# Kernel optimization log

Hardware: AMD Instinct MI355X
Metric: run time of the kernel (lower is better)

The kernel has to match this reference:

```python
import jax, jax.numpy as jnp
import numpy as np

B, D, P, K = 16384, 2048, 64, 5


def setup_inputs() -> dict:
    key = jax.random.key(0)
    k1, k2, k3, k4, k5 = jax.random.split(key, 5)
    s = 1.0 / np.sqrt(D)
    return {
        "x": jax.random.normal(k1, (B, D), dtype=jnp.float32),
        "parent_W": jax.random.normal(k2, (P, D), dtype=jnp.float32) * s,
        "parent_b": jax.random.normal(k3, (P,), dtype=jnp.float32) * s,
        "child_W": jax.random.normal(k4, (P, K, D), dtype=jnp.float32) * s,
        "child_b": jax.random.normal(k5, (P, K), dtype=jnp.float32) * s,
    }


def reference(x, parent_W, parent_b, child_W, child_b):
    # Parent linear: [B, P]
    parent_logits = x @ parent_W.T + parent_b
    # softmax is monotonic, so argmax(softmax(l)) == argmax(l)
    parent_class = jnp.argmax(parent_logits, axis=1)  # [B] int
    # Gather each sample's expert (child classifier) weights: [B, K, D], [B, K]
    Wc = child_W[parent_class]
    bc = child_b[parent_class]
    # Per-sample tiny GEMM, batched: [B, K]
    child_logits = jnp.einsum("bd,bkd->bk", x, Wc) + bc
    return parent_logits, child_logits
```

## Files before the change

### kernel.cpp

```cpp
#include <hip/hip_runtime.h>

#define B_ 16384
#define D_ 2048
#define P_ 64
#define K_ 5

#define BK 64
#define NCH (D_ / BK)
#define LDR 72
#define SPLIT_SC 2048.0f
#define SPLIT_INV (1.0f / 2048.0f)

typedef _Float16 half8 __attribute__((ext_vector_type(8)));
typedef float f32x4 __attribute__((ext_vector_type(4)));

static __device__ __forceinline__ void split8(const float4 a, const float4 b,
                                              half8& hi, half8& lo) {
  const float v[8] = {a.x, a.y, a.z, a.w, b.x, b.y, b.z, b.w};
#pragma unroll
  for (int i = 0; i < 8; ++i) {
    const _Float16 h = (_Float16)v[i];
    hi[i] = h;
    lo[i] = (_Float16)((v[i] - (float)h) * SPLIT_SC);
  }
}

__global__ __launch_bounds__(256) void k1_parent(
    const float* __restrict__ x, const float* __restrict__ pW,
    const float* __restrict__ pb, float* __restrict__ pout,
    int* __restrict__ cnt, int* __restrict__ list) {
  __shared__ _Float16 xlh[2][64 * LDR], xll[2][64 * LDR];
  __shared__ _Float16 wlh[2][64 * LDR], wll[2][64 * LDR];
  __shared__ float rmax[64][4];
  __shared__ int ridx[64][4];

  const int tid = threadIdx.x;
  const int b0 = blockIdx.x * 64;
  const int w = tid >> 6;
  const int l = tid & 63;
  const int r = tid >> 2;
  const int c = tid & 3;

  const float* xg = x + (size_t)(b0 + r) * D_ + c * 16;
  const float* wg = pW + (size_t)r * D_ + c * 16;
  const float bias = pb[w * 16 + (l & 15)];

  const int aoff = (l & 15) * LDR + (l >> 4) * 8;
  const int boff = (w * 16 + (l & 15)) * LDR + (l >> 4) * 8;
  const int soff = r * LDR + c * 16;

  f32x4 acc[4], accc[4];
#pragma unroll
  for (int fm = 0; fm < 4; ++fm) {
    acc[fm] = {0.f, 0.f, 0.f, 0.f};
    accc[fm] = {0.f, 0.f, 0.f, 0.f};
  }

  {
    const float4* xp = (const float4*)xg;
    const float4* wp = (const float4*)wg;
    half8 h, lo;
    split8(xp[0], xp[1], h, lo);
    *(half8*)&xlh[0][soff] = h; *(half8*)&xll[0][soff] = lo;
    split8(xp[2], xp[3], h, lo);
    *(half8*)&xlh[0][soff + 8] = h; *(half8*)&xll[0][soff + 8] = lo;
    split8(wp[0], wp[1], h, lo);
    *(half8*)&wlh[0][soff] = h; *(half8*)&wll[0][soff] = lo;
    split8(wp[2], wp[3], h, lo);
    *(half8*)&wlh[0][soff + 8] = h; *(half8*)&wll[0][soff + 8] = lo;
  }
  __syncthreads();

  for (int ch = 0; ch < NCH; ++ch) {
    const int cur = ch & 1;
    float4 x0, x1, x2, x3, w0, w1, w2, w3;
    const bool more = (ch + 1 < NCH);
    if (more) {
      const float4* xp = (const float4*)(xg + (ch + 1) * BK);
      const float4* wp = (const float4*)(wg + (ch + 1) * BK);
      x0 = xp[0]; x1 = xp[1]; x2 = xp[2]; x3 = xp[3];
      w0 = wp[0]; w1 = wp[1]; w2 = wp[2]; w3 = wp[3];
    }
#pragma unroll
    for (int s = 0; s < 2; ++s) {
      const int ko = s * 32;
      const half8 bh = *(const half8*)&wlh[cur][boff + ko];
      const half8 bl = *(const half8*)&wll[cur][boff + ko];
#pragma unroll
      for (int fm = 0; fm < 4; ++fm) {
        const half8 ah = *(const half8*)&xlh[cur][aoff + fm * 16 * LDR + ko];
        const half8 al = *(const half8*)&xll[cur][aoff + fm * 16 * LDR + ko];
        acc[fm]  = __builtin_amdgcn_mfma_f32_16x16x32_f16(ah, bh, acc[fm], 0, 0, 0);
        accc[fm] = __builtin_amdgcn_mfma_f32_16x16x32_f16(ah, bl, accc[fm], 0, 0, 0);
        accc[fm] = __builtin_amdgcn_mfma_f32_16x16x32_f16(al, bh, accc[fm], 0, 0, 0);
      }
    }
    if (more) {
      const int nxt = cur ^ 1;
      half8 h, lo;
      split8(x0, x1, h, lo);
      *(half8*)&xlh[nxt][soff] = h; *(half8*)&xll[nxt][soff] = lo;
      split8(x2, x3, h, lo);
      *(half8*)&xlh[nxt][soff + 8] = h; *(half8*)&xll[nxt][soff + 8] = lo;
      split8(w0, w1, h, lo);
      *(half8*)&wlh[nxt][soff] = h; *(half8*)&wll[nxt][soff] = lo;
      split8(w2, w3, h, lo);
      *(half8*)&wlh[nxt][soff + 8] = h; *(half8*)&wll[nxt][soff + 8] = lo;
    }
    __syncthreads();
  }

  const int colbase = w * 16 + (l & 15);
  float val[4][4];
#pragma unroll
  for (int fm = 0; fm < 4; ++fm) {
#pragma unroll
    for (int j = 0; j < 4; ++j) {
      val[fm][j] = acc[fm][j] + accc[fm][j] * SPLIT_INV + bias;
      const int row = fm * 16 + ((l >> 4) << 2) + j;
      pout[(size_t)(b0 + row) * P_ + colbase] = val[fm][j];
    }
  }
#pragma unroll
  for (int fm = 0; fm < 4; ++fm) {
#pragma unroll
    for (int j = 0; j < 4; ++j) {
      float bv = val[fm][j];
      int bi = colbase;
#pragma unroll
      for (int s = 8; s > 0; s >>= 1) {
        const float ov = __shfl_xor(bv, s, 64);
        const int oi = __shfl_xor(bi, s, 64);
        if (ov > bv || (ov == bv && oi < bi)) { bv = ov; bi = oi; }
      }
      if ((l & 15) == 0) {
        const int row = fm * 16 + ((l >> 4) << 2) + j;
        rmax[row][w] = bv;
        ridx[row][w] = bi;
      }
    }
  }
  __syncthreads();
  if (tid < 64) {
    float bv = rmax[tid][0];
    int bi = ridx[tid][0];
#pragma unroll
    for (int ww = 1; ww < 4; ++ww) {
      const float ov = rmax[tid][ww];
      const int oi = ridx[tid][ww];
      if (ov > bv || (ov == bv && oi < bi)) { bv = ov; bi = oi; }
    }
    const int slot = atomicAdd(&cnt[bi * 16], 1);
    if (slot < 1024) list[bi * 1024 + slot] = b0 + tid;
  }
}

__global__ __launch_bounds__(256) void k2_child(const float* __restrict__ x,
                                                const float* __restrict__ cW,
                                                const float* __restrict__ cb,
                                                const int* __restrict__ cnt,
                                                const int* __restrict__ list,
                                                float* __restrict__ cout) {
  __shared__ float wlds[K_ * D_];
  const int e = blockIdx.x >> 2;
  const int chk = blockIdx.x & 3;
  const int tid = threadIdx.x;

  const float4* wg4 = (const float4*)(cW + (size_t)e * (K_ * D_));
  float4* wl4 = (float4*)wlds;
#pragma unroll
  for (int tI = 0; tI < 10; ++tI) wl4[tid + 256 * tI] = wg4[tid + 256 * tI];
  __syncthreads();

  const int n = min(cnt[e * 16], 1024);
  const int per = (n + 3) >> 2;
  const int lo = chk * per;
  const int hi = min(lo + per, n);
  const int m = hi - lo;
  if (m <= 0) return;

  const int wave = tid >> 6, lane = tid & 63;
  const int wper = (m + 3) >> 2;
  const int wlo = lo + wave * wper;
  const int whi = min(wlo + wper, hi);

  const float4* x4 = (const float4*)x;
  const int* mylist = list + e * 1024;

  for (int i0 = wlo; i0 < whi; i0 += 4) {
    const int vb = min(4, whi - i0);
    const int ra = mylist[i0];
    const int rb = mylist[i0 + min(1, vb - 1)];
    const int rc = mylist[i0 + min(2, vb - 1)];
    const int rd = mylist[i0 + min(3, vb - 1)];

    float a[20];
#pragma unroll
    for (int q = 0; q < 20; ++q) a[q] = 0.f;

#pragma unroll
    for (int tt = 0; tt < 8; ++tt) {
      const float4 xv0 = x4[(size_t)ra * 512 + lane + 64 * tt];
      const float4 xv1 = x4[(size_t)rb * 512 + lane + 64 * tt];
      const float4 xv2 = x4[(size_t)rc * 512 + lane + 64 * tt];
      const float4 xv3 = x4[(size_t)rd * 512 + lane + 64 * tt];
#pragma unroll
      for (int k = 0; k < 5; ++k) {
        const float4 wv = wl4[k * 512 + lane + 64 * tt];
        a[0 * 5 + k] += xv0.x * wv.x + xv0.y * wv.y + xv0.z * wv.z + xv0.w * wv.w;
        a[1 * 5 + k] += xv1.x * wv.x + xv1.y * wv.y + xv1.z * wv.z + xv1.w * wv.w;
        a[2 * 5 + k] += xv2.x * wv.x + xv2.y * wv.y + xv2.z * wv.z + xv2.w * wv.w;
        a[3 * 5 + k] += xv3.x * wv.x + xv3.y * wv.y + xv3.z * wv.z + xv3.w * wv.w;
      }
    }
#pragma unroll
    for (int p = 0; p < 10; ++p) {
      float va = a[2 * p], vb2 = a[2 * p + 1];
      va += __shfl_xor(va, 32, 64);
      vb2 += __shfl_xor(vb2, 32, 64);
      float z = (lane < 32) ? va : vb2;
      z += __shfl_xor(z, 16, 64);
      z += __shfl_xor(z, 8, 64);
      z += __shfl_xor(z, 4, 64);
      z += __shfl_xor(z, 2, 64);
      z += __shfl_xor(z, 1, 64);
      a[2 * p] = z;
    }
    if (lane == 0 || lane == 32) {
      const int off = (lane == 32) ? 1 : 0;
#pragma unroll
      for (int p = 0; p < 10; ++p) {
        const int f = 2 * p + off;
        const int rr = f / 5, kk = f % 5;
        if (rr < vb) {
          const int rX = (rr == 0) ? ra : (rr == 1) ? rb : (rr == 2) ? rc : rd;
          cout[(size_t)rX * K_ + kk] = a[2 * p] + cb[e * K_ + kk];
        }
      }
    }
  }
}

extern "C" void kernel_launch(void* const* d_in, const int* in_sizes, int n_in,
                              void* d_out, int out_size, void* d_ws, size_t ws_size,
                              hipStream_t stream) {
  const float* x  = (const float*)d_in[0];
  const float* pW = (const float*)d_in[1];
  const float* pb = (const float*)d_in[2];
  const float* cW = (const float*)d_in[3];
  const float* cb = (const float*)d_in[4];
  float* pout = (float*)d_out;
  float* cout = (float*)d_out + (size_t)B_ * P_;

  char* ws = (char*)d_ws;
  int* cnt  = (int*)ws;
  int* list = (int*)(ws + 4096);

  hipMemsetAsync(cnt, 0, 4096, stream);
  k1_parent<<<B_ / 64, 256, 0, stream>>>(x, pW, pb, pout, cnt, list);
  k2_child<<<P_ * 4, 256, 0, stream>>>(x, cW, cb, cnt, list, cout);
}
```

Before: 268.9 us.

## Pre-split parent weights once, shrink parent tiles, widen child grid

After: 286.1 us. +6.4%, slower.

```diff
diff --git a/kernel.cpp b/kernel.cpp
--- a/kernel.cpp
+++ b/kernel.cpp
@@ -12,136 +12,120 @@
 #define SPLIT_INV (1.0f / 2048.0f)
 
 typedef _Float16 half8 __attribute__((ext_vector_type(8)));
+typedef _Float16 half4 __attribute__((ext_vector_type(4)));
 typedef float f32x4 __attribute__((ext_vector_type(4)));
 
-static __device__ __forceinline__ void split8(const float4 a, const float4 b,
-                                              half8& hi, half8& lo) {
-  const float v[8] = {a.x, a.y, a.z, a.w, b.x, b.y, b.z, b.w};
-#pragma unroll
-  for (int i = 0; i < 8; ++i) {
-    const _Float16 h = (_Float16)v[i];
+static __device__ __forceinline__ void split4(const float4 v, half4& hi, half4& lo) {
+  const float f[4] = {v.x, v.y, v.z, v.w};
+#pragma unroll
+  for (int i = 0; i < 4; ++i) {
+    const _Float16 h = (_Float16)f[i];
     hi[i] = h;
-    lo[i] = (_Float16)((v[i] - (float)h) * SPLIT_SC);
-  }
+    lo[i] = (_Float16)((f[i] - (float)h) * SPLIT_SC);
+  }
+}
+
+__global__ __launch_bounds__(256) void k0_split(const float* __restrict__ W,
+                                                _Float16* __restrict__ whi,
+                                                _Float16* __restrict__ wlo) {
+  const int i = (blockIdx.x * 256 + threadIdx.x) * 4;
+  const float4 v = *(const float4*)&W[i];
+  half4 h, lo;
+  split4(v, h, lo);
+  *(half4*)&whi[i] = h;
+  *(half4*)&wlo[i] = lo;
 }
 
 __global__ __launch_bounds__(256) void k1_parent(
-    const float* __restrict__ x, const float* __restrict__ pW,
-    const float* __restrict__ pb, float* __restrict__ pout,
-    int* __restrict__ cnt, int* __restrict__ list) {
-  __shared__ _Float16 xlh[2][64 * LDR], xll[2][64 * LDR];
-  __shared__ _Float16 wlh[2][64 * LDR], wll[2][64 * LDR];
-  __shared__ float rmax[64][4];
-  __shared__ int ridx[64][4];
+    const float* __restrict__ x, const _Float16* __restrict__ whi,
+    const _Float16* __restrict__ wlo, const float* __restrict__ pb,
+    float* __restrict__ pout, int* __restrict__ cnt, int* __restrict__ list) {
+  __shared__ _Float16 xlh[2][16 * LDR], xll[2][16 * LDR];
+  __shared__ float rmax[16][4];
+  __shared__ int ridx[16][4];
 
   const int tid = threadIdx.x;
-  const int b0 = blockIdx.x * 64;
+  const int b0 = blockIdx.x * 16;
   const int w = tid >> 6;
   const int l = tid & 63;
-  const int r = tid >> 2;
-  const int c = tid & 3;
-
-  const float* xg = x + (size_t)(b0 + r) * D_ + c * 16;
-  const float* wg = pW + (size_t)r * D_ + c * 16;
+  const int sr = tid >> 4;
+  const int sc = tid & 15;
+
+  const float* xg = x + (size_t)(b0 + sr) * D_ + sc * 4;
   const float bias = pb[w * 16 + (l & 15)];
 
   const int aoff = (l & 15) * LDR + (l >> 4) * 8;
-  const int boff = (w * 16 + (l & 15)) * LDR + (l >> 4) * 8;
-  const int soff = r * LDR + c * 16;
-
-  f32x4 acc[4], accc[4];
-#pragma unroll
-  for (int fm = 0; fm < 4; ++fm) {
-    acc[fm] = {0.f, 0.f, 0.f, 0.f};
-    accc[fm] = {0.f, 0.f, 0.f, 0.f};
-  }
+  const int soff = sr * LDR + sc * 4;
+  const _Float16* bhp = whi + (size_t)(w * 16 + (l & 15)) * D_ + (l >> 4) * 8;
+  const _Float16* blp = wlo + (size_t)(w * 16 + (l & 15)) * D_ + (l >> 4) * 8;
+
+  f32x4 acc = {0.f, 0.f, 0.f, 0.f}, accc = {0.f, 0.f, 0.f, 0.f};
 
   {
-    const float4* xp = (const float4*)xg;
-    const float4* wp = (const float4*)wg;
-    half8 h, lo;
-    split8(xp[0], xp[1], h, lo);
-    *(half8*)&xlh[0][soff] = h; *(half8*)&xll[0][soff] = lo;
-    split8(xp[2], xp[3], h, lo);
-    *(half8*)&xlh[0][soff + 8] = h; *(half8*)&xll[0][soff + 8] = lo;
-    split8(wp[0], wp[1], h, lo);
-    *(half8*)&wlh[0][soff] = h; *(half8*)&wll[0][soff] = lo;
-    split8(wp[2], wp[3], h, lo);
-    *(half8*)&wlh[0][soff + 8] = h; *(half8*)&wll[0][soff + 8] = lo;
+    const float4 v = *(const float4*)xg;
+    half4 h, lo;
+    split4(v, h, lo);
+    *(half4*)&xlh[0][soff] = h;
+    *(half4*)&xll[0][soff] = lo;
   }
   __syncthreads();
 
   for (int ch = 0; ch < NCH; ++ch) {
     const int cur = ch & 1;
-    float4 x0, x1, x2, x3, w0, w1, w2, w3;
     const bool more = (ch + 1 < NCH);
+    float4 xv;
+    if (more) xv = *(const float4*)(xg + (ch + 1) * BK);
+
+    const half8 bh0 = *(const half8*)&bhp[ch * BK];
+    const half8 bl0 = *(const half8*)&blp[ch * BK];
+    const half8 bh1 = *(const half8*)&bhp[ch * BK + 32];
+    const half8 bl1 = *(const half8*)&blp[ch * BK + 32];
+    const half8 ah0 = *(const half8*)&xlh[cur][aoff];
+    const half8 al0 = *(const half8*)&xll[cur][aoff];
+    const half8 ah1 = *(const half8*)&xlh[cur][aoff + 32];
+    const half8 al1 = *(const half8*)&xll[cur][aoff + 32];
+
+    acc  = __builtin_amdgcn_mfma_f32_16x16x32_f16(ah0, bh0, acc, 0, 0, 0);
+    accc = __builtin_amdgcn_mfma_f32_16x16x32_f16(ah0, bl0, accc, 0, 0, 0);
+    accc = __builtin_amdgcn_mfma_f32_16x16x32_f16(al0, bh0, accc, 0, 0, 0);
+    acc  = __builtin_amdgcn_mfma_f32_16x16x32_f16(ah1, bh1, acc, 0, 0, 0);
+    accc = __builtin_amdgcn_mfma_f32_16x16x32_f16(ah1, bl1, accc, 0, 0, 0);
+    accc = __builtin_amdgcn_mfma_f32_16x16x32_f16(al1, bh1, accc, 0, 0, 0);
+
     if (more) {
-      const float4* xp = (const float4*)(xg + (ch + 1) * BK);
-      const float4* wp = (const float4*)(wg + (ch + 1) * BK);
-      x0 = xp[0]; x1 = xp[1]; x2 = xp[2]; x3 = xp[3];
-      w0 = wp[0]; w1 = wp[1]; w2 = wp[2]; w3 = wp[3];
-    }
-#pragma unroll
-    for (int s = 0; s < 2; ++s) {
-      const int ko = s * 32;
-      const half8 bh = *(const half8*)&wlh[cur][boff + ko];
-      const half8 bl = *(const half8*)&wll[cur][boff + ko];
-#pragma unroll
-      for (int fm = 0; fm < 4; ++fm) {
-        const half8 ah = *(const half8*)&xlh[cur][aoff + fm * 16 * LDR + ko];
-        const half8 al = *(const half8*)&xll[cur][aoff + fm * 16 * LDR + ko];
-        acc[fm]  = __builtin_amdgcn_mfma_f32_16x16x32_f16(ah, bh, acc[fm], 0, 0, 0);
-        accc[fm] = __builtin_amdgcn_mfma_f32_16x16x32_f16(ah, bl, accc[fm], 0, 0, 0);
-        accc[fm] = __builtin_amdgcn_mfma_f32_16x16x32_f16(al, bh, accc[fm], 0, 0, 0);
-      }
-    }
-    if (more) {
-      const int nxt = cur ^ 1;
-      half8 h, lo;
-      split8(x0, x1, h, lo);
-      *(half8*)&xlh[nxt][soff] = h; *(half8*)&xll[nxt][soff] = lo;
-      split8(x2, x3, h, lo);
-      *(half8*)&xlh[nxt][soff + 8] = h; *(half8*)&xll[nxt][soff + 8] = lo;
-      split8(w0, w1, h, lo);
-      *(half8*)&wlh[nxt][soff] = h; *(half8*)&wll[nxt][soff] = lo;
-      split8(w2, w3, h, lo);
-      *(half8*)&wlh[nxt][soff + 8] = h; *(half8*)&wll[nxt][soff + 8] = lo;
+      half4 h, lo;
+      split4(xv, h, lo);
+      *(half4*)&xlh[cur ^ 1][soff] = h;
+      *(half4*)&xll[cur ^ 1][soff] = lo;
     }
     __syncthreads();
   }
 
   const int colbase = w * 16 + (l & 15);
-  float val[4][4];
-#pragma unroll
-  for (int fm = 0; fm < 4; ++fm) {
-#pragma unroll
-    for (int j = 0; j < 4; ++j) {
-      val[fm][j] = acc[fm][j] + accc[fm][j] * SPLIT_INV + bias;
-      const int row = fm * 16 + ((l >> 4) << 2) + j;
-      pout[(size_t)(b0 + row) * P_ + colbase] = val[fm][j];
-    }
-  }
-#pragma unroll
-  for (int fm = 0; fm < 4; ++fm) {
-#pragma unroll
-    for (int j = 0; j < 4; ++j) {
-      float bv = val[fm][j];
-      int bi = colbase;
-#pragma unroll
-      for (int s = 8; s > 0; s >>= 1) {
-        const float ov = __shfl_xor(bv, s, 64);
-        const int oi = __shfl_xor(bi, s, 64);
-        if (ov > bv || (ov == bv && oi < bi)) { bv = ov; bi = oi; }
-      }
-      if ((l & 15) == 0) {
-        const int row = fm * 16 + ((l >> 4) << 2) + j;
-        rmax[row][w] = bv;
-        ridx[row][w] = bi;
-      }
+  float val[4];
+#pragma unroll
+  for (int j = 0; j < 4; ++j) {
+    val[j] = acc[j] + accc[j] * SPLIT_INV + bias;
+    const int row = ((l >> 4) << 2) + j;
+    pout[(size_t)(b0 + row) * P_ + colbase] = val[j];
+  }
+#pragma unroll
+  for (int j = 0; j < 4; ++j) {
+    float bv = val[j];
+    int bi = colbase;
+#pragma unroll
+    for (int s = 8; s > 0; s >>= 1) {
+      const float ov = __shfl_xor(bv, s, 64);
+      const int oi = __shfl_xor(bi, s, 64);
+      if (ov > bv || (ov == bv && oi < bi)) { bv = ov; bi = oi; }
+    }
+    if ((l & 15) == 0) {
+      rmax[((l >> 4) << 2) + j][w] = bv;
+      ridx[((l >> 4) << 2) + j][w] = bi;
     }
   }
   __syncthreads();
-  if (tid < 64) {
+  if (tid < 16) {
     float bv = rmax[tid][0];
     int bi = ridx[tid][0];
 #pragma unroll
@@ -162,8 +146,8 @@
                                                 const int* __restrict__ list,
                                                 float* __restrict__ cout) {
   __shared__ float wlds[K_ * D_];
-  const int e = blockIdx.x >> 2;
-  const int chk = blockIdx.x & 3;
+  const int e = blockIdx.x >> 4;
+  const int chk = blockIdx.x & 15;
   const int tid = threadIdx.x;
 
   const float4* wg4 = (const float4*)(cW + (size_t)e * (K_ * D_));
@@ -173,7 +157,7 @@
   __syncthreads();
 
   const int n = min(cnt[e * 16], 1024);
-  const int per = (n + 3) >> 2;
+  const int per = (n + 15) >> 4;
   const int lo = chk * per;
   const int hi = min(lo + per, n);
   const int m = hi - lo;
@@ -182,13 +166,13 @@
   const int wave = tid >> 6, lane = tid & 63;
   const int wper = (m + 3) >> 2;
   const int wlo = lo + wave * wper;
-  const int whi = min(wlo + wper, hi);
+  const int whi_ = min(wlo + wper, hi);
 
   const float4* x4 = (const float4*)x;
   const int* mylist = list + e * 1024;
 
-  for (int i0 = wlo; i0 < whi; i0 += 4) {
-    const int vb = min(4, whi - i0);
+  for (int i0 = wlo; i0 < whi_; i0 += 4) {
+    const int vb = min(4, whi_ - i0);
     const int ra = mylist[i0];
     const int rb = mylist[i0 + min(1, vb - 1)];
     const int rc = mylist[i0 + min(2, vb - 1)];
@@ -253,10 +237,13 @@
   float* cout = (float*)d_out + (size_t)B_ * P_;
 
   char* ws = (char*)d_ws;
-  int* cnt  = (int*)ws;
-  int* list = (int*)(ws + 4096);
+  _Float16* whi = (_Float16*)ws;
+  _Float16* wlo = (_Float16*)(ws + 262144);
+  int* cnt  = (int*)(ws + 524288);
+  int* list = (int*)(ws + 528384);
 
   hipMemsetAsync(cnt, 0, 4096, stream);
-  k1_parent<<<B_ / 64, 256, 0, stream>>>(x, pW, pb, pout, cnt, list);
-  k2_child<<<P_ * 4, 256, 0, stream>>>(x, cW, cb, cnt, list, cout);
-}
+  k0_split<<<128, 256, 0, stream>>>(pW, whi, wlo);
+  k1_parent<<<B_ / 16, 256, 0, stream>>>(x, whi, wlo, pb, pout, cnt, list);
+  k2_child<<<P_ * 16, 256, 0, stream>>>(x, cW, cb, cnt, list, cout);
+}
```
